# Performance work log

Hardware: AMD Instinct MI355X
Metric: run time of the kernel (lower is better)

## Reference

```python
import jax, jax.numpy as jnp
import numpy as np

B = 8192       # batch
HID = 1024     # hidden_dim
HEADS = 8      # head_count
OBS, ACT, N_AGENTS = 128, 32, 4
ENC_IN = N_AGENTS * OBS + ACT   # 544
DEC_IN = (N_AGENTS - 1) * ACT   # 96


def _linear(key, fan_in, fan_out):
    k1, k2 = jax.random.split(key)
    lim = 1.0 / np.sqrt(fan_in)
    W = jax.random.uniform(k1, (fan_in, fan_out), minval=-lim, maxval=lim, dtype=jnp.float32)
    b = jax.random.uniform(k2, (fan_out,), minval=-lim, maxval=lim, dtype=jnp.float32)
    return W, b


def setup_inputs() -> dict:
    key = jax.random.key(0)
    ks = jax.random.split(key, 10)
    s = jax.random.normal(ks[0], (B, N_AGENTS * OBS), dtype=jnp.float32)
    a = jax.random.normal(ks[1], (B, N_AGENTS * ACT), dtype=jnp.float32)
    W_enc_in, b_enc_in = _linear(ks[2], ENC_IN, HID)   # encoder_input_fc
    W_dec_in, b_dec_in = _linear(ks[3], DEC_IN, HID)   # decoder_input_fc
    W_eh, b_eh = _linear(ks[4], HID, HID)              # fc_encoder_input
    head_ks = jax.random.split(ks[5], HEADS)
    Wb = [_linear(k, HID, HID) for k in head_ks]       # fc_encoder_heads
    W_heads = jnp.stack([w for w, _ in Wb], axis=0)    # [H, HID, HID]
    b_heads = jnp.stack([b for _, b in Wb], axis=0)    # [H, HID]
    W_dh, b_dh = _linear(ks[6], HID, HID)              # fc_decoder_input
    W1, b1 = _linear(ks[7], HID, HID)                  # fc1
    W2, b2 = _linear(ks[8], HID, 1)                    # fc2
    return {"s": s, "a": a,
            "W_enc_in": W_enc_in, "b_enc_in": b_enc_in,
            "W_dec_in": W_dec_in, "b_dec_in": b_dec_in,
            "W_eh": W_eh, "b_eh": b_eh,
            "W_heads": W_heads, "b_heads": b_heads,
            "W_dh": W_dh, "b_dh": b_dh,
            "W1": W1, "b1": b1, "W2": W2, "b2": b2}


def reference(s, a, W_enc_in, b_enc_in, W_dec_in, b_dec_in, W_eh, b_eh,
              W_heads, b_heads, W_dh, b_dh, W1, b1, W2, b2):
    relu = jax.nn.relu
    # agent id = 0: own action is a[:, :ACT], others' actions are a[:, ACT:]
    enc_input = jnp.concatenate([s, a[:, :ACT]], axis=1) @ W_enc_in + b_enc_in   # [B, HID]
    dec_input = a[:, ACT:] @ W_dec_in + b_dec_in                                 # [B, HID]
    # Attention_ATT_2
    encoder_h = relu(enc_input @ W_eh + b_eh)                                    # [B, HID]
    encoder_heads = relu(jnp.einsum('bd,hde->hbe', encoder_h, W_heads)
                         + b_heads[:, None, :])                                  # [H, B, HID]
    decoder_H = relu(dec_input @ W_dh + b_dh)                                    # [B, HID]
    scores = jnp.einsum('hbd,bd->bh', encoder_heads, decoder_H)                  # [B, H]
    attn = jax.nn.softmax(scores, axis=1)                                        # [B, H]
    context = jnp.einsum('hbd,bh->bd', encoder_heads, attn)                      # [B, HID]
    x = relu(context @ W1 + b1)
    q = x @ W2 + b2                                                              # [B, 1]
    return q
```

## Files before the change

### kernel.cpp

```cpp
#include <hip/hip_runtime.h>
#include <hip/hip_bf16.h>
#include <hip/hip_fp16.h>

#define BATCH   8192
#define HID     1024
#define HEADS   8
#define BC      2048

typedef unsigned int  u32;
typedef unsigned short u16;
typedef __attribute__((ext_vector_type(8))) short bf16x8;
typedef __attribute__((ext_vector_type(4))) float f32x4;
typedef __attribute__((ext_vector_type(16))) float f32x16;

__device__ __forceinline__ u32 pack_hi2(u32 u0, u32 u1) {
    return (u0 >> 16) | (u1 & 0xFFFF0000u);
}
__device__ __forceinline__ void split1(float x, u16& h, u16& l) {
    const u32 u = __float_as_uint(x);
    h = (u16)(u >> 16);
    const float r = x - __uint_as_float(u & 0xFFFF0000u);
    l = (u16)(__float_as_uint(r) >> 16);
}
__device__ __forceinline__ void splitA4(float4 v, uint2& hi, uint2& lo) {
    u32 u0 = __float_as_uint(v.x), u1 = __float_as_uint(v.y),
        u2 = __float_as_uint(v.z), u3 = __float_as_uint(v.w);
    float r0 = v.x - __uint_as_float(u0 & 0xFFFF0000u);
    float r1 = v.y - __uint_as_float(u1 & 0xFFFF0000u);
    float r2 = v.z - __uint_as_float(u2 & 0xFFFF0000u);
    float r3 = v.w - __uint_as_float(u3 & 0xFFFF0000u);
    hi.x = pack_hi2(u0, u1);
    hi.y = pack_hi2(u2, u3);
    lo.x = pack_hi2(__float_as_uint(r0), __float_as_uint(r1));
    lo.y = pack_hi2(__float_as_uint(r2), __float_as_uint(r3));
}

__device__ __forceinline__ void gld16(const u16* g, u16* l) {
    __builtin_amdgcn_global_load_lds(
        (const __attribute__((address_space(1))) u32*)g,
        (__attribute__((address_space(3))) u32*)l, 16, 0, 0);
}

struct WSplitArgs {
    const float* src[6];
    u16* hi[6];
    u16* lo[6];
};

__global__ __launch_bounds__(256) void split_weight_all(WSplitArgs args)
{
    const int z = blockIdx.z;
    int which, zz = 0;
    if (z < 3)       { which = z; }
    else if (z < 11) { which = 3; zz = z - 3; }
    else             { which = z - 7; }
    const int KT = (which == 4) ? 17 : (which == 5 ? 3 : 32);
    const int kt = blockIdx.x;
    if (kt >= KT) return;
    const int K = KT * 32;
    const long long zoff = (long long)zz * K * 1024;
    const float* W  = args.src[which] + zoff;
    u16* hi = args.hi[which] + zoff;
    u16* lo = args.lo[which] + zoff;

    const int n0  = blockIdx.y * 128;
    const int tid = threadIdx.x;
    const int k   = tid >> 3;
    const int ng  = (tid & 7) * 16;
    const float* src = W + (long long)(kt * 32 + k) * 1024 + n0 + ng;
    u16* dh = hi + ((long long)kt * 1024 + n0) * 32 + k;
    u16* dl = lo + ((long long)kt * 1024 + n0) * 32 + k;
#pragma unroll
    for (int t = 0; t < 4; t++) {
        const float4 v = *(const float4*)(src + t * 4);
        u16 h0, l0, h1, l1, h2, l2, h3, l3;
        split1(v.x, h0, l0); split1(v.y, h1, l1);
        split1(v.z, h2, l2); split1(v.w, h3, l3);
        const int nb = (ng + t * 4) * 32;
        dh[nb]      = h0; dl[nb]      = l0;
        dh[nb + 32] = h1; dl[nb + 32] = l1;
        dh[nb + 64] = h2; dl[nb + 64] = l2;
        dh[nb + 96] = h3; dl[nb + 96] = l3;
    }
}

#define MFMA32_GEOM \
    const int tid  = threadIdx.x; \
    const int lane = tid & 63; \
    const int wv   = tid >> 6; \
    const int wm   = wv >> 1, wn = wv & 1; \
    const int c    = lane & 31; \
    const int hh   = lane >> 5; \
    const int cs   = c & 3; \
    const int m0   = blockIdx.y * 128; \
    const int n0   = blockIdx.x * 128; \
    const int lro  = (lane >> 2) * 32 + (((lane & 3) ^ ((lane >> 2) & 3)) * 8); \
    const int br0  = wv * 16; \
    const int br1  = 64 + wv * 16;

#define STAGE8(Ahp_, Alp_, Bhp_, Blp_, aoff_, boff_) \
    { \
        const u16* Ag_  = (Ahp_) + (aoff_); \
        const u16* Ag2_ = (Alp_) + (aoff_); \
        const u16* Bg_  = (Bhp_) + (boff_); \
        const u16* Bg2_ = (Blp_) + (boff_); \
        gld16(Ag_  + br0 * 32 + lro, &Ah[br0 * 32]); \
        gld16(Ag_  + br1 * 32 + lro, &Ah[br1 * 32]); \
        gld16(Ag2_ + br0 * 32 + lro, &Al[br0 * 32]); \
        gld16(Ag2_ + br1 * 32 + lro, &Al[br1 * 32]); \
        gld16(Bg_  + br0 * 32 + lro, &Bh[br0 * 32]); \
        gld16(Bg_  + br1 * 32 + lro, &Bh[br1 * 32]); \
        gld16(Bg2_ + br0 * 32 + lro, &Bl[br0 * 32]); \
        gld16(Bg2_ + br1 * 32 + lro, &Bl[br1 * 32]); \
    }

#define MFMA32_SLAB(accv) \
    _Pragma("unroll") \
    for (int s = 0; s < 2; s++) { \
        bf16x8 av0[2], av1[2], bv0[2], bv1[2]; \
        const int ko = ((s * 2 + hh) ^ cs) * 8; \
        _Pragma("unroll") \
        for (int t = 0; t < 2; t++) { \
            const int ao = (wm * 64 + t * 32 + c) * 32 + ko; \
            const int bo = (wn * 64 + t * 32 + c) * 32 + ko; \
            av0[t] = *(const bf16x8*)&Ah[ao]; \
            av1[t] = *(const bf16x8*)&Al[ao]; \
            bv0[t] = *(const bf16x8*)&Bh[bo]; \
            bv1[t] = *(const bf16x8*)&Bl[bo]; \
        } \
        _Pragma("unroll") \
        for (int i = 0; i < 2; i++) \
            _Pragma("unroll") \
            for (int j = 0; j < 2; j++) { \
                accv[i][j] = __builtin_amdgcn_mfma_f32_32x32x16_bf16(av0[i], bv0[j], accv[i][j], 0, 0, 0); \
                accv[i][j] = __builtin_amdgcn_mfma_f32_32x32x16_bf16(av0[i], bv1[j], accv[i][j], 0, 0, 0); \
                accv[i][j] = __builtin_amdgcn_mfma_f32_32x32x16_bf16(av1[i], bv0[j], accv[i][j], 0, 0, 0); \
            } \
    }

template <int RELU, int OUTP>
__global__ __launch_bounds__(256) void gemm_fast(
    const u16* __restrict__ Ahp, const u16* __restrict__ Alp, int MA, int moff,
    const u16* __restrict__ Bhp, const u16* __restrict__ Blp,
    const float* __restrict__ bias,
    float* __restrict__ Cf,
    u16* __restrict__ Chp, u16* __restrict__ Clp, int MC,
    int K)
{
    __shared__ alignas(16) u16 Ah[4096], Al[4096], Bh[4096], Bl[4096];
    MFMA32_GEOM

    f32x16 acc[2][2];
    acc[0][0] = 0; acc[0][1] = 0; acc[1][0] = 0; acc[1][1] = 0;

    const int KT = K >> 5;
    for (int kt = 0; kt < KT; kt++) {
        STAGE8(Ahp, Alp, Bhp, Blp,
               ((long long)kt * MA + moff + m0) * 32,
               ((long long)kt * 1024 + n0) * 32);
        __syncthreads();
        MFMA32_SLAB(acc);
        __syncthreads();
    }

#pragma unroll
    for (int j = 0; j < 2; j++) {
        const int n = n0 + wn * 64 + j * 32 + c;
        const float bb = bias[n];
#pragma unroll
        for (int i = 0; i < 2; i++) {
#pragma unroll
            for (int reg = 0; reg < 16; reg++) {
                const int m = m0 + wm * 64 + i * 32 + 4 * hh + (reg & 3) + 8 * (reg >> 2);
                float v = acc[i][j][reg] + bb;
                if (RELU) v = fmaxf(v, 0.0f);
                if (OUTP) {
                    u16 h, l;
                    split1(v, h, l);
                    const long long d = ((long long)(n >> 5) * MC + moff + m) * 32 + (n & 31);
                    Chp[d] = h;
                    Clp[d] = l;
                } else {
                    Cf[(long long)m * 1024 + n] = v;
                }
            }
        }
    }
}

template <int RELU>
__global__ __launch_bounds__(256) void gemm_cvt(
    const float* __restrict__ src1, int lda1, int kofs1,
    const float* __restrict__ src2, int lda2, int ksplit,
    const u16* __restrict__ Bhp, const u16* __restrict__ Blp,
    const float* __restrict__ bias,
    u16* __restrict__ Chp, u16* __restrict__ Clp, int MC,
    int K)
{
    __shared__ alignas(16) u16 Ah[4096], Al[4096], Bh[4096], Bl[4096];
    const int tid  = threadIdx.x;
    const int lane = tid & 63;
    const int wv   = tid >> 6;
    const int wm   = wv >> 1, wn = wv & 1;
    const int fr   = lane & 15;
    const int fq   = lane >> 4;
    const int m0   = blockIdx.y * 128;
    const int n0   = blockIdx.x * 128;
    const int fqx  = (fq ^ (fr & 3)) * 8;
    const int lro  = (lane >> 2) * 32 + (((lane & 3) ^ ((lane >> 2) & 3)) * 8);
    const int br0  = wv * 16;
    const int br1  = 64 + wv * 16;
    const int ar   = tid >> 3;
    const int akq  = tid & 7;
    const int awoff = (((akq >> 1) ^ (ar & 3)) * 8) + (akq & 1) * 4;

    f32x4 acc[4][4];
#pragma unroll
    for (int i = 0; i < 4; i++)
#pragma unroll
        for (int j = 0; j < 4; j++) acc[i][j] = 0;

    const int KT = K >> 5;
    for (int kt = 0; kt < KT; kt++) {
        const int k0 = kt * 32;
        const float* srcp; int ldk, kc;
        if (k0 < ksplit) { srcp = src1; ldk = lda1; kc = k0 + kofs1; }
        else             { srcp = src2; ldk = lda2; kc = k0 - ksplit; }

        const u16* Bg  = Bhp + ((long long)kt * 1024 + n0) * 32;
        const u16* Bg2 = Blp + ((long long)kt * 1024 + n0) * 32;
        gld16(Bg  + br0 * 32 + lro, &Bh[br0 * 32]);
        gld16(Bg  + br1 * 32 + lro, &Bh[br1 * 32]);
        gld16(Bg2 + br0 * 32 + lro, &Bl[br0 * 32]);
        gld16(Bg2 + br1 * 32 + lro, &Bl[br1 * 32]);

#pragma unroll
        for (int it = 0; it < 4; it++) {
            const int row = ar + it * 32;
            const float4 v = *(const float4*)(srcp + (long long)(m0 + row) * ldk + kc + akq * 4);
            uint2 hi, lo;
            splitA4(v, hi, lo);
            *(uint2*)&Ah[row * 32 + awoff] = hi;
            *(uint2*)&Al[row * 32 + awoff] = lo;
        }
        __syncthreads();

        bf16x8 ah[4], al[4], bh[4], bl[4];
#pragma unroll
        for (int i = 0; i < 4; i++) {
            const int off = (wm * 64 + i * 16 + fr) * 32 + fqx;
            ah[i] = *(const bf16x8*)&Ah[off];
            al[i] = *(const bf16x8*)&Al[off];
        }
#pragma unroll
        for (int j = 0; j < 4; j++) {
            const int off = (wn * 64 + j * 16 + fr) * 32 + fqx;
            bh[j] = *(const bf16x8*)&Bh[off];
            bl[j] = *(const bf16x8*)&Bl[off];
        }
#pragma unroll
        for (int i = 0; i < 4; i++)
#pragma unroll
            for (int j = 0; j < 4; j++) {
                acc[i][j] = __builtin_amdgcn_mfma_f32_16x16x32_bf16(ah[i], bh[j], acc[i][j], 0, 0, 0);
                acc[i][j] = __builtin_amdgcn_mfma_f32_16x16x32_bf16(ah[i], bl[j], acc[i][j], 0, 0, 0);
                acc[i][j] = __builtin_amdgcn_mfma_f32_16x16x32_bf16(al[i], bh[j], acc[i][j], 0, 0, 0);
            }
        __syncthreads();
    }

#pragma unroll
    for (int j = 0; j < 4; j++) {
        const int n = n0 + wn * 64 + j * 16 + fr;
        const float bb = bias[n];
#pragma unroll
        for (int i = 0; i < 4; i++) {
#pragma unroll
            for (int r = 0; r < 4; r++) {
                const int m = m0 + wm * 64 + i * 16 + fq * 4 + r;
                float v = acc[i][j][r] + bb;
                if (RELU) v = fmaxf(v, 0.0f);
                u16 h, l;
                split1(v, h, l);
                const long long d = ((long long)(n >> 5) * MC + m) * 32 + (n & 31);
                Chp[d] = h;
                Clp[d] = l;
            }
        }
    }
}

__global__ __launch_bounds__(256) void heads_kernel(
    const u16* __restrict__ Ahp, const u16* __restrict__ Alp, int MA, int moff,
    const u16* __restrict__ Whp, const u16* __restrict__ Wlp,
    const float* __restrict__ b_heads,
    const float* __restrict__ decH,
    __half* __restrict__ headsb,
    float* __restrict__ scoresp)
{
    __shared__ alignas(16) u16 Ah[4096], Al[4096], Bh[4096], Bl[4096];
    __shared__ float scred[2][128];
    MFMA32_GEOM
    const int h = blockIdx.z;
    const u16* Bhp = Whp + (long long)h * 1048576;
    const u16* Blp = Wlp + (long long)h * 1048576;
    const float* bias = b_heads + h * 1024;

    f32x16 acc[2][2];
    acc[0][0] = 0; acc[0][1] = 0; acc[1][0] = 0; acc[1][1] = 0;

    for (int kt = 0; kt < 32; kt++) {
        STAGE8(Ahp, Alp, Bhp, Blp,
               ((long long)kt * MA + moff + m0) * 32,
               ((long long)kt * 1024 + n0) * 32);
        __syncthreads();
        MFMA32_SLAB(acc);
        __syncthreads();
    }

    float part[2][16];
#pragma unroll
    for (int i = 0; i < 2; i++)
#pragma unroll
        for (int reg = 0; reg < 16; reg++) part[i][reg] = 0.0f;

#pragma unroll
    for (int j = 0; j < 2; j++) {
        const int n = n0 + wn * 64 + j * 32 + c;
        const float bb = bias[n];
#pragma unroll
        for (int i = 0; i < 2; i++) {
#pragma unroll
            for (int reg = 0; reg < 16; reg++) {
                const int b_loc = m0 + wm * 64 + i * 32 + 4 * hh + (reg & 3) + 8 * (reg >> 2);
                const float v = fmaxf(acc[i][j][reg] + bb, 0.0f);
                headsb[((long long)b_loc * HEADS + h) * 1024 + n] = __float2half(v);
                part[i][reg] = fmaf(v, decH[(long long)b_loc * 1024 + n], part[i][reg]);
            }
        }
    }
#pragma unroll
    for (int off = 1; off < 32; off <<= 1)
#pragma unroll
        for (int i = 0; i < 2; i++)
#pragma unroll
            for (int reg = 0; reg < 16; reg++)
                part[i][reg] += __shfl_xor(part[i][reg], off, 64);

    if (c == 0) {
#pragma unroll
        for (int i = 0; i < 2; i++)
#pragma unroll
            for (int reg = 0; reg < 16; reg++)
                scred[wn][wm * 64 + i * 32 + 4 * hh + (reg & 3) + 8 * (reg >> 2)] = part[i][reg];
    }
    __syncthreads();
    if (tid < 128) {
        const float sv = scred[0][tid] + scred[1][tid];
        scoresp[(long long)(h * 8 + blockIdx.x) * BC + m0 + tid] = sv;
    }
}

__global__ __launch_bounds__(256) void context_kernel(
    const __half* __restrict__ headsb, const float* __restrict__ scoresp,
    u16* __restrict__ ctx_hi, u16* __restrict__ ctx_lo, int MC, int row0)
{
    __shared__ float sc_s[64];
    __shared__ float attn_s[HEADS];
    const int b = blockIdx.x;
    const int tid = threadIdx.x;
    if (tid < 64) sc_s[tid] = scoresp[(long long)tid * BC + b];
    __syncthreads();
    if (tid == 0) {
        float sc[HEADS];
#pragma unroll
        for (int h = 0; h < HEADS; h++) {
            float s = 0.0f;
#pragma unroll
            for (int nt = 0; nt < 8; nt++) s += sc_s[h * 8 + nt];
            sc[h] = s;
        }
        float mx = sc[0];
#pragma unroll
        for (int h = 1; h < HEADS; h++) mx = fmaxf(mx, sc[h]);
        float e[HEADS], sum = 0.0f;
#pragma unroll
        for (int h = 0; h < HEADS; h++) { e[h] = __expf(sc[h] - mx); sum += e[h]; }
        const float inv = 1.0f / sum;
#pragma unroll
        for (int h = 0; h < HEADS; h++) attn_s[h] = e[h] * inv;
    }
    __syncthreads();

    const int d = tid * 4;
    float w[HEADS];
#pragma unroll
    for (int h = 0; h < HEADS; h++) w[h] = attn_s[h];
    float4 acc = make_float4(0.f, 0.f, 0.f, 0.f);
#pragma unroll
    for (int h = 0; h < HEADS; h++) {
        const __half2* hp = (const __half2*)(headsb + ((long long)b * HEADS + h) * 1024 + d);
        const float2 f0 = __half22float2(hp[0]);
        const float2 f1 = __half22float2(hp[1]);
        acc.x = fmaf(w[h], f0.x, acc.x);
        acc.y = fmaf(w[h], f0.y, acc.y);
        acc.z = fmaf(w[h], f1.x, acc.z);
        acc.w = fmaf(w[h], f1.y, acc.w);
    }
    uint2 hi, lo;
    splitA4(acc, hi, lo);
    const long long off = ((long long)(d >> 5) * MC + row0 + b) * 32 + (d & 31);
    *(uint2*)(ctx_hi + off) = hi;
    *(uint2*)(ctx_lo + off) = lo;
}

__global__ __launch_bounds__(256) void fc2_kernel(
    const float* __restrict__ x, const float* __restrict__ W2,
    const float* __restrict__ b2, float* __restrict__ q)
{
    const int b   = blockIdx.x;
    const int tid = threadIdx.x;
    __shared__ float red[4];

    const float4 xv = *(const float4*)(x + (long long)b * 1024 + tid * 4);
    const float4 wv = *(const float4*)(W2 + tid * 4);
    float p = xv.x * wv.x + xv.y * wv.y + xv.z * wv.z + xv.w * wv.w;
#pragma unroll
    for (int off = 32; off > 0; off >>= 1) p += __shfl_down(p, off, 64);
    if ((tid & 63) == 0) red[tid >> 6] = p;
    __syncthreads();
    if (tid == 0) q[b] = red[0] + red[1] + red[2] + red[3] + b2[0];
}

extern "C" void kernel_launch(void* const* d_in, const int* in_sizes, int n_in,
                              void* d_out, int out_size, void* d_ws, size_t ws_size,
                              hipStream_t stream)
{
    const float* s        = (const float*)d_in[0];
    const float* a        = (const float*)d_in[1];
    const float* W_enc_in = (const float*)d_in[2];
    const float* b_enc_in = (const float*)d_in[3];
    const float* W_dec_in = (const float*)d_in[4];
    const float* b_dec_in = (const float*)d_in[5];
    const float* W_eh     = (const float*)d_in[6];
    const float* b_eh     = (const float*)d_in[7];
    const float* W_heads  = (const float*)d_in[8];
    const float* b_heads  = (const float*)d_in[9];
    const float* W_dh     = (const float*)d_in[10];
    const float* b_dh     = (const float*)d_in[11];
    const float* W1       = (const float*)d_in[12];
    const float* b1       = (const float*)d_in[13];
    const float* W2       = (const float*)d_in[14];
    const float* b2       = (const float*)d_in[15];
    float* q_out = (float*)d_out;

    u16* P = (u16*)d_ws;
    u16* enc_hi = P; P += 557056;
    u16* enc_lo = P; P += 557056;
    u16* dec_hi = P; P += 98304;
    u16* dec_lo = P; P += 98304;
    u16* eh_hi  = P; P += 1048576;
    u16* eh_lo  = P; P += 1048576;
    u16* dh_hi  = P; P += 1048576;
    u16* dh_lo  = P; P += 1048576;
    u16* w1_hi  = P; P += 1048576;
    u16* w1_lo  = P; P += 1048576;
    u16* wh_hi  = P; P += 8388608;
    u16* wh_lo  = P; P += 8388608;
    char* act = (char*)P;

    const dim3 blk(256);

    WSplitArgs wa;
    wa.src[0] = W_eh;    wa.hi[0] = eh_hi;  wa.lo[0] = eh_lo;
    wa.src[1] = W_dh;    wa.hi[1] = dh_hi;  wa.lo[1] = dh_lo;
    wa.src[2] = W1;      wa.hi[2] = w1_hi;  wa.lo[2] = w1_lo;
    wa.src[3] = W_heads; wa.hi[3] = wh_hi;  wa.lo[3] = wh_lo;
    wa.src[4] = W_enc_in; wa.hi[4] = enc_hi; wa.lo[4] = enc_lo;
    wa.src[5] = W_dec_in; wa.hi[5] = dec_hi; wa.lo[5] = dec_lo;
    split_weight_all<<<dim3(32, 8, 13), blk, 0, stream>>>(wa);

    const bool high = (ws_size >= 150011904ULL);

    if (high) {
        u16*    bufA_hi = (u16*)act;
        u16*    bufA_lo = bufA_hi + 8388608;
        __half* headsb  = (__half*)act;
        u16*    encH_hi = (u16*)(act + 33554432);
        u16*    encH_lo = encH_hi + 8388608;
        float*  decH    = (float*)(act + 2LL * 33554432);
        float*  scoresp = (float*)(act + 3LL * 33554432);

        const dim3 gg(8, 64, 1);
        gemm_cvt<0><<<gg, blk, 0, stream>>>(s, 512, 0, a, 128, 512,
            enc_hi, enc_lo, b_enc_in, bufA_hi, bufA_lo, 8192, 544);
        gemm_fast<1, 1><<<gg, blk, 0, stream>>>(bufA_hi, bufA_lo, 8192, 0,
            eh_hi, eh_lo, b_eh, nullptr, encH_hi, encH_lo, 8192, 1024);
        gemm_cvt<0><<<gg, blk, 0, stream>>>(a, 128, 32, a, 128, 1 << 28,
            dec_hi, dec_lo, b_dec_in, bufA_hi, bufA_lo, 8192, 96);
        gemm_fast<1, 0><<<gg, blk, 0, stream>>>(bufA_hi, bufA_lo, 8192, 0,
            dh_hi, dh_lo, b_dh, decH, nullptr, nullptr, 0, 1024);

        for (int c = 0; c < BATCH / BC; c++) {
            heads_kernel<<<dim3(8, BC / 128, 8), blk, 0, stream>>>(
                encH_hi, encH_lo, 8192, c * BC, wh_hi, wh_lo, b_heads,
                decH + (long long)c * BC * 1024, headsb, scoresp);
            context_kernel<<<dim3(BC), blk, 0, stream>>>(
                headsb, scoresp, encH_hi, encH_lo, 8192, c * BC);
        }
        gemm_fast<1, 0><<<gg, blk, 0, stream>>>(encH_hi, encH_lo, 8192, 0,
            w1_hi, w1_lo, b1, decH, nullptr, nullptr, 0, 1024);
        fc2_kernel<<<dim3(BATCH), blk, 0, stream>>>(decH, W2, b2, q_out);
    } else {
        __half* headsb  = (__half*)act;
        u16*    bufA_hi = (u16*)act;
        u16*    bufA_lo = bufA_hi + 2097152;
        u16*    encH_hi = (u16*)(act + 33554432);
        u16*    encH_lo = encH_hi + 2097152;
        float*  decH    = (float*)(act + 33554432 + 8388608);
        float*  scoresp = (float*)(act + 33554432 + 2LL * 8388608);

        const dim3 gg(8, BC / 128, 1);
        for (int c = 0; c < BATCH / BC; c++) {
            const float* sC = s + (long long)c * BC * 512;
            const float* aC = a + (long long)c * BC * 128;
            gemm_cvt<0><<<gg, blk, 0, stream>>>(sC, 512, 0, aC, 128, 512,
                enc_hi, enc_lo, b_enc_in, bufA_hi, bufA_lo, BC, 544);
            gemm_fast<1, 1><<<gg, blk, 0, stream>>>(bufA_hi, bufA_lo, BC, 0,
                eh_hi, eh_lo, b_eh, nullptr, encH_hi, encH_lo, BC, 1024);
            gemm_cvt<0><<<gg, blk, 0, stream>>>(aC, 128, 32, aC, 128, 1 << 28,
                dec_hi, dec_lo, b_dec_in, bufA_hi, bufA_lo, BC, 96);
            gemm_fast<1, 0><<<gg, blk, 0, stream>>>(bufA_hi, bufA_lo, BC, 0,
                dh_hi, dh_lo, b_dh, decH, nullptr, nullptr, 0, 1024);
            heads_kernel<<<dim3(8, BC / 128, 8), blk, 0, stream>>>(
                encH_hi, encH_lo, BC, 0, wh_hi, wh_lo, b_heads,
                decH, headsb, scoresp);
            context_kernel<<<dim3(BC), blk, 0, stream>>>(
                headsb, scoresp, encH_hi, encH_lo, BC, 0);
            gemm_fast<1, 0><<<gg, blk, 0, stream>>>(encH_hi, encH_lo, BC, 0,
                w1_hi, w1_lo, b1, decH, nullptr, nullptr, 0, 1024);
            fc2_kernel<<<dim3(BC), blk, 0, stream>>>(decH, W2, b2, q_out + (long long)c * BC);
        }
    }
}
```

Measured before the change: 840.9 us.

## Switch to 16x16x32 MFMA and load low-part fragments directly to registers

Replaces the 32x32x16 bf16 MFMA tiling with 16x16x32 MFMAs in a 4x4 accumulator grid per wave. Only the high bf16 parts of A and B are staged through shared memory. The low-part fragments are loaded straight from global memory into registers, since each is used by only one wave. This halves LDS footprint and traffic and changes the swizzle. In exchange, uncoalesced-ish direct global loads for the lo parts sit on the critical path before the barrier, and the epilogue reduction layout changes.

Result: faster. 807.3 us (-4.0%).

```diff
diff --git a/kernel.cpp b/kernel.cpp
--- a/kernel.cpp
+++ b/kernel.cpp
@@ -11,7 +11,6 @@
 typedef unsigned short u16;
 typedef __attribute__((ext_vector_type(8))) short bf16x8;
 typedef __attribute__((ext_vector_type(4))) float f32x4;
-typedef __attribute__((ext_vector_type(16))) float f32x16;
 
 __device__ __forceinline__ u32 pack_hi2(u32 u0, u32 u1) {
     return (u0 >> 16) | (u1 & 0xFFFF0000u);
@@ -84,57 +83,56 @@
     }
 }
 
-#define MFMA32_GEOM \
+#define HYB_GEOM \
     const int tid  = threadIdx.x; \
     const int lane = tid & 63; \
     const int wv   = tid >> 6; \
     const int wm   = wv >> 1, wn = wv & 1; \
-    const int c    = lane & 31; \
-    const int hh   = lane >> 5; \
-    const int cs   = c & 3; \
+    const int fr   = lane & 15; \
+    const int fq   = lane >> 4; \
     const int m0   = blockIdx.y * 128; \
     const int n0   = blockIdx.x * 128; \
-    const int lro  = (lane >> 2) * 32 + (((lane & 3) ^ ((lane >> 2) & 3)) * 8); \
+    const int lro2 = (lane >> 2) * 32 + (((lane & 3) ^ ((lane >> 3) & 3)) * 8); \
     const int br0  = wv * 16; \
-    const int br1  = 64 + wv * 16;
-
-#define STAGE8(Ahp_, Alp_, Bhp_, Blp_, aoff_, boff_) \
+    const int br1  = 64 + wv * 16; \
+    const int fqx2 = (fq ^ ((fr >> 1) & 3)) * 8;
+
+#define STAGE_HI(Ahp_, Bhp_, aoff_, boff_) \
     { \
-        const u16* Ag_  = (Ahp_) + (aoff_); \
-        const u16* Ag2_ = (Alp_) + (aoff_); \
-        const u16* Bg_  = (Bhp_) + (boff_); \
-        const u16* Bg2_ = (Blp_) + (boff_); \
-        gld16(Ag_  + br0 * 32 + lro, &Ah[br0 * 32]); \
-        gld16(Ag_  + br1 * 32 + lro, &Ah[br1 * 32]); \
-        gld16(Ag2_ + br0 * 32 + lro, &Al[br0 * 32]); \
-        gld16(Ag2_ + br1 * 32 + lro, &Al[br1 * 32]); \
-        gld16(Bg_  + br0 * 32 + lro, &Bh[br0 * 32]); \
-        gld16(Bg_  + br1 * 32 + lro, &Bh[br1 * 32]); \
-        gld16(Bg2_ + br0 * 32 + lro, &Bl[br0 * 32]); \
-        gld16(Bg2_ + br1 * 32 + lro, &Bl[br1 * 32]); \
-    }
-
-#define MFMA32_SLAB(accv) \
-    _Pragma("unroll") \
-    for (int s = 0; s < 2; s++) { \
-        bf16x8 av0[2], av1[2], bv0[2], bv1[2]; \
-        const int ko = ((s * 2 + hh) ^ cs) * 8; \
+        const u16* Ag_ = (Ahp_) + (aoff_); \
+        const u16* Bg_ = (Bhp_) + (boff_); \
+        gld16(Ag_ + br0 * 32 + lro2, &Ah[br0 * 32]); \
+        gld16(Ag_ + br1 * 32 + lro2, &Ah[br1 * 32]); \
+        gld16(Bg_ + br0 * 32 + lro2, &Bh[br0 * 32]); \
+        gld16(Bg_ + br1 * 32 + lro2, &Bh[br1 * 32]); \
+    }
+
+#define LOAD_LO(Alp_, Blp_, aoff_, boff_, al_, bl_) \
+    { \
+        const u16* Al_ = (Alp_) + (aoff_); \
+        const u16* Bl_ = (Blp_) + (boff_); \
         _Pragma("unroll") \
-        for (int t = 0; t < 2; t++) { \
-            const int ao = (wm * 64 + t * 32 + c) * 32 + ko; \
-            const int bo = (wn * 64 + t * 32 + c) * 32 + ko; \
-            av0[t] = *(const bf16x8*)&Ah[ao]; \
-            av1[t] = *(const bf16x8*)&Al[ao]; \
-            bv0[t] = *(const bf16x8*)&Bh[bo]; \
-            bv1[t] = *(const bf16x8*)&Bl[bo]; \
+        for (int i = 0; i < 4; i++) { \
+            al_[i] = *(const bf16x8*)(Al_ + (wm * 64 + i * 16 + fr) * 32 + fq * 8); \
+            bl_[i] = *(const bf16x8*)(Bl_ + (wn * 64 + i * 16 + fr) * 32 + fq * 8); \
+        } \
+    }
+
+#define MFMA_SLAB16(acc_, al_, bl_) \
+    { \
+        bf16x8 ah[4], bh[4]; \
+        _Pragma("unroll") \
+        for (int i = 0; i < 4; i++) { \
+            ah[i] = *(const bf16x8*)&Ah[(wm * 64 + i * 16 + fr) * 32 + fqx2]; \
+            bh[i] = *(const bf16x8*)&Bh[(wn * 64 + i * 16 + fr) * 32 + fqx2]; \
         } \
         _Pragma("unroll") \
-        for (int i = 0; i < 2; i++) \
+        for (int i = 0; i < 4; i++) \
             _Pragma("unroll") \
-            for (int j = 0; j < 2; j++) { \
-                accv[i][j] = __builtin_amdgcn_mfma_f32_32x32x16_bf16(av0[i], bv0[j], accv[i][j], 0, 0, 0); \
-                accv[i][j] = __builtin_amdgcn_mfma_f32_32x32x16_bf16(av0[i], bv1[j], accv[i][j], 0, 0, 0); \
-                accv[i][j] = __builtin_amdgcn_mfma_f32_32x32x16_bf16(av1[i], bv0[j], accv[i][j], 0, 0, 0); \
+            for (int j = 0; j < 4; j++) { \
+                acc_[i][j] = __builtin_amdgcn_mfma_f32_16x16x32_bf16(ah[i], bh[j], acc_[i][j], 0, 0, 0); \
+                acc_[i][j] = __builtin_amdgcn_mfma_f32_16x16x32_bf16(ah[i], bl_[j], acc_[i][j], 0, 0, 0); \
+                acc_[i][j] = __builtin_amdgcn_mfma_f32_16x16x32_bf16(al_[i], bh[j], acc_[i][j], 0, 0, 0); \
             } \
     }
 
@@ -147,32 +145,37 @@
     u16* __restrict__ Chp, u16* __restrict__ Clp, int MC,
     int K)
 {
-    __shared__ alignas(16) u16 Ah[4096], Al[4096], Bh[4096], Bl[4096];
-    MFMA32_GEOM
-
-    f32x16 acc[2][2];
-    acc[0][0] = 0; acc[0][1] = 0; acc[1][0] = 0; acc[1][1] = 0;
+    __shared__ alignas(16) u16 Ah[4096], Bh[4096];
+    HYB_GEOM
+
+    f32x4 acc[4][4];
+#pragma unroll
+    for (int i = 0; i < 4; i++)
+#pragma unroll
+        for (int j = 0; j < 4; j++) acc[i][j] = 0;
 
     const int KT = K >> 5;
     for (int kt = 0; kt < KT; kt++) {
-        STAGE8(Ahp, Alp, Bhp, Blp,
-               ((long long)kt * MA + moff + m0) * 32,
-               ((long long)kt * 1024 + n0) * 32);
+        const long long aoff = ((long long)kt * MA + moff + m0) * 32;
+        const long long boff = ((long long)kt * 1024 + n0) * 32;
+        STAGE_HI(Ahp, Bhp, aoff, boff);
+        bf16x8 al[4], bl[4];
+        LOAD_LO(Alp, Blp, aoff, boff, al, bl);
         __syncthreads();
-        MFMA32_SLAB(acc);
+        MFMA_SLAB16(acc, al, bl);
         __syncthreads();
     }
 
 #pragma unroll
-    for (int j = 0; j < 2; j++) {
-        const int n = n0 + wn * 64 + j * 32 + c;
+    for (int j = 0; j < 4; j++) {
+        const int n = n0 + wn * 64 + j * 16 + fr;
         const float bb = bias[n];
 #pragma unroll
-        for (int i = 0; i < 2; i++) {
-#pragma unroll
-            for (int reg = 0; reg < 16; reg++) {
-                const int m = m0 + wm * 64 + i * 32 + 4 * hh + (reg & 3) + 8 * (reg >> 2);
-                float v = acc[i][j][reg] + bb;
+        for (int i = 0; i < 4; i++) {
+#pragma unroll
+            for (int r = 0; r < 4; r++) {
+                const int m = m0 + wm * 64 + i * 16 + fq * 4 + r;
+                float v = acc[i][j][r] + bb;
                 if (RELU) v = fmaxf(v, 0.0f);
                 if (OUTP) {
                     u16 h, l;
@@ -298,61 +301,66 @@
     __half* __restrict__ headsb,
     float* __restrict__ scoresp)
 {
-    __shared__ alignas(16) u16 Ah[4096], Al[4096], Bh[4096], Bl[4096];
+    __shared__ alignas(16) u16 Ah[4096], Bh[4096];
     __shared__ float scred[2][128];
-    MFMA32_GEOM
+    HYB_GEOM
     const int h = blockIdx.z;
     const u16* Bhp = Whp + (long long)h * 1048576;
     const u16* Blp = Wlp + (long long)h * 1048576;
     const float* bias = b_heads + h * 1024;
 
-    f32x16 acc[2][2];
-    acc[0][0] = 0; acc[0][1] = 0; acc[1][0] = 0; acc[1][1] = 0;
+    f32x4 acc[4][4];
+#pragma unroll
+    for (int i = 0; i < 4; i++)
+#pragma unroll
+        for (int j = 0; j < 4; j++) acc[i][j] = 0;
 
     for (int kt = 0; kt < 32; kt++) {
-        STAGE8(Ahp, Alp, Bhp, Blp,
-               ((long long)kt * MA + moff + m0) * 32,
-               ((long long)kt * 1024 + n0) * 32);
+        const long long aoff = ((long long)kt * MA + moff + m0) * 32;
+        const long long boff = ((long long)kt * 1024 + n0) * 32;
+        STAGE_HI(Ahp, Bhp, aoff, boff);
+        bf16x8 al[4], bl[4];
+        LOAD_LO(Alp, Blp, aoff, boff, al, bl);
         __syncthreads();
-        MFMA32_SLAB(acc);
+        MFMA_SLAB16(acc, al, bl);
         __syncthreads();
     }
 
-    float part[2][16];
-#pragma unroll
-    for (int i = 0; i < 2; i++)
-#pragma unroll
-        for (int reg = 0; reg < 16; reg++) part[i][reg] = 0.0f;
-
-#pragma unroll
-    for (int j = 0; j < 2; j++) {
-        const int n = n0 + wn * 64 + j * 32 + c;
+    float part[4][4];
+#pragma unroll
+    for (int i = 0; i < 4; i++)
+#pragma unroll
+        for (int r = 0; r < 4; r++) part[i][r] = 0.0f;
+
+#pragma unroll
+    for (int j = 0; j < 4; j++) {
+        const int n = n0 + wn * 64 + j * 16 + fr;
         const float bb = bias[n];
 #pragma unroll
-        for (int i = 0; i < 2; i++) {
-#pragma unroll
-            for (int reg = 0; reg < 16; reg++) {
-                const int b_loc = m0 + wm * 64 + i * 32 + 4 * hh + (reg & 3) + 8 * (reg >> 2);
-                const float v = fmaxf(acc[i][j][reg] + bb, 0.0f);
+        for (int i = 0; i < 4; i++) {
+#pragma unroll
+            for (int r = 0; r < 4; r++) {
+                const int b_loc = m0 + wm * 64 + i * 16 + fq * 4 + r;
+                const float v = fmaxf(acc[i][j][r] + bb, 0.0f);
                 headsb[((long long)b_loc * HEADS + h) * 1024 + n] = __float2half(v);
-                part[i][reg] = fmaf(v, decH[(long long)b_loc * 1024 + n], part[i][reg]);
+                part[i][r] = fmaf(v, decH[(long long)b_loc * 1024 + n], part[i][r]);
             }
         }
     }
 #pragma unroll
-    for (int off = 1; off < 32; off <<= 1)
-#pragma unroll
-        for (int i = 0; i < 2; i++)
-#pragma unroll
-            for (int reg = 0; reg < 16; reg++)
-                part[i][reg] += __shfl_xor(part[i][reg], off, 64);
-
-    if (c == 0) {
-#pragma unroll
-        for (int i = 0; i < 2; i++)
-#pragma unroll
-            for (int reg = 0; reg < 16; reg++)
-                scred[wn][wm * 64 + i * 32 + 4 * hh + (reg & 3) + 8 * (reg >> 2)] = part[i][reg];
+    for (int off = 1; off < 16; off <<= 1)
+#pragma unroll
+        for (int i = 0; i < 4; i++)
+#pragma unroll
+            for (int r = 0; r < 4; r++)
+                part[i][r] += __shfl_xor(part[i][r], off, 64);
+
+    if (fr == 0) {
+#pragma unroll
+        for (int i = 0; i < 4; i++)
+#pragma unroll
+            for (int r = 0; r < 4; r++)
+                scred[wn][wm * 64 + i * 16 + fq * 4 + r] = part[i][r];
     }
     __syncthreads();
     if (tid < 128) {
```
